# Kernel tuning notes

Measured on AMD Instinct MI355X. Metric: run time of the kernel, lower is better.

## Reference

```python
import jax, jax.numpy as jnp
import numpy as np
from jax import lax

B, T = 2048, 256
H1, H2 = 51, 51


def _cell(x, h, c, w_ih, w_hh, b_ih, b_hh):
    # PyTorch LSTMCell math: gates = x W_ih^T + h W_hh^T + b_ih + b_hh
    gates = x @ w_ih.T + h @ w_hh.T + (b_ih + b_hh)
    i, f, g, o = jnp.split(gates, 4, axis=-1)
    c2 = jax.nn.sigmoid(f) * c + jax.nn.sigmoid(i) * jnp.tanh(g)
    h2 = jax.nn.sigmoid(o) * jnp.tanh(c2)
    return h2, c2


def setup_inputs() -> dict:
    key = jax.random.key(0)
    ks = jax.random.split(key, 17)
    s1 = 1.0 / np.sqrt(H1)
    s4 = 1.0  # hidden size 1 -> bound 1
    def u(k, shape, s):
        return jax.random.uniform(k, shape, jnp.float32, -s, s)
    return {
        "input": jax.random.normal(ks[0], (B, T), jnp.float32),
        "w_ih1": u(ks[1], (4 * H1, 1), s1), "w_hh1": u(ks[2], (4 * H1, H1), s1),
        "b_ih1": u(ks[3], (4 * H1,), s1), "b_hh1": u(ks[4], (4 * H1,), s1),
        "w_ih2": u(ks[5], (4 * H2, H1), s1), "w_hh2": u(ks[6], (4 * H2, H2), s1),
        "b_ih2": u(ks[7], (4 * H2,), s1), "b_hh2": u(ks[8], (4 * H2,), s1),
        "w_ih3": u(ks[9], (4 * H1, H2), s1), "w_hh3": u(ks[10], (4 * H1, H1), s1),
        "b_ih3": u(ks[11], (4 * H1,), s1), "b_hh3": u(ks[12], (4 * H1,), s1),
        "w_ih4": u(ks[13], (4, H1), s4), "w_hh4": u(ks[14], (4, 1), s4),
        "b_ih4": u(ks[15], (4,), s4), "b_hh4": u(ks[16], (4,), s4),
    }


def reference(input, w_ih1, w_hh1, b_ih1, b_hh1, w_ih2, w_hh2, b_ih2, b_hh2,
              w_ih3, w_hh3, b_ih3, b_hh3, w_ih4, w_hh4, b_ih4, b_hh4):
    b = input.shape[0]
    z = lambda d: jnp.zeros((b, d), input.dtype)
    init = (z(H1), z(H1), z(H2), z(H2), z(H1), z(H1), z(1), z(1))

    def stack(x, carry):
        h1, c1, h2, c2, h3, c3, h4, c4 = carry
        h1, c1 = _cell(x, h1, c1, w_ih1, w_hh1, b_ih1, b_hh1)
        # quirk of the original module: cell states feed the next layer
        h2, c2 = _cell(c1, h2, c2, w_ih2, w_hh2, b_ih2, b_hh2)
        h3, c3 = _cell(c2, h3, c3, w_ih3, w_hh3, b_ih3, b_hh3)
        h4, c4 = _cell(c3, h4, c4, w_ih4, w_hh4, b_ih4, b_hh4)
        return (h1, c1, h2, c2, h3, c3, h4, c4)

    def step(carry, x_t):
        return stack(x_t, carry), None

    xs = input.T[:, :, None]  # [T, B, 1]
    carry, _ = lax.scan(step, init, xs)
    # extra step: feed final c4 back as the input
    carry = stack(carry[7], carry)
    return carry[7]  # final cell state of lstm4, shape [B, 1]
```

## Files before the change

### kernel.cpp

```cpp
#include <hip/hip_runtime.h>


typedef _Float16 f16x8 __attribute__((ext_vector_type(8)));
typedef float    f32x4 __attribute__((ext_vector_type(4)));

constexpr int BATCH   = 2048;
constexpr int T_STEPS = 256;
constexpr int H   = 51;
constexpr int NTILE = 13;
constexpr int NUNIT = 5 * NTILE * 2 + 2;
constexpr int XKP = 80;

__device__ __forceinline__ float frcp(float x) { return __builtin_amdgcn_rcpf(x); }
__device__ __forceinline__ float sigmoid_f(float x) { float e = __expf(-x); return frcp(1.f + e); }
__device__ __forceinline__ float tanh_f(float x) {
    float e = __expf(2.f * x);
    return 1.f - 2.f * frcp(e + 1.f);
}

#define PIN16(x) { f32x4 _t = __builtin_bit_cast(f32x4, x); asm volatile("" : "+v"(_t)); x = __builtin_bit_cast(f16x8, _t); }
#define PIN4(x)  asm volatile("" : "+v"(x))

__global__ __launch_bounds__(256) void prep_mfma(
    const float* __restrict__ w_ih1, const float* __restrict__ w_hh1,
    const float* __restrict__ w_ih2, const float* __restrict__ w_hh2,
    const float* __restrict__ w_ih3, const float* __restrict__ w_hh3,
    const float* __restrict__ w_ih4, _Float16* __restrict__ wpa)
{
    int id = blockIdx.x * 256 + threadIdx.x;
    if (id >= NUNIT * 64) return;
    int u = id >> 6, l = id & 63;
    int row16 = l & 15;
    int kbase = ((u & 1) ? 32 : 0) + ((l >> 4) << 3);
    f16x8 v;
    if (u < 130) {
        int pm = u / 26, tile = (u % 26) >> 1;
        const float* W = (pm == 0) ? w_hh1 : (pm == 1) ? w_ih2 : (pm == 2) ? w_hh2
                       : (pm == 3) ? w_ih3 : w_hh3;
        int kh = tile * 4 + (row16 >> 2);
        int q  = row16 & 3;
        bool rv = (kh < H);
        int orow = q * H + kh;
#pragma unroll
        for (int e = 0; e < 8; ++e) {
            int j = kbase + e;
            float val = 0.f;
            if (rv) {
                if (j < H)                  val = W[orow * H + j];
                else if (j == H && pm == 0) val = w_ih1[orow];
            }
            v[e] = (_Float16)val;
        }
    } else {
#pragma unroll
        for (int e = 0; e < 8; ++e) {
            int j = kbase + e;
            v[e] = (_Float16)((row16 < 4 && j < H) ? w_ih4[row16 * H + j] : 0.f);
        }
    }
    *(f16x8*)(wpa + (size_t)u * 512 + l * 8) = v;
}

__global__ __launch_bounds__(512, 2) void lstm4_main(
    const float* __restrict__ input, const _Float16* __restrict__ wpa,
    const float* __restrict__ b_ih1, const float* __restrict__ b_hh1,
    const float* __restrict__ b_ih2, const float* __restrict__ b_hh2,
    const float* __restrict__ b_ih3, const float* __restrict__ b_hh3,
    const float* __restrict__ w_hh4,
    const float* __restrict__ b_ih4, const float* __restrict__ b_hh4,
    float* __restrict__ out)
{
    __shared__ __align__(16) _Float16 xh[6][2][8][XKP];
    __shared__ float inl[8 * 260];

    const int tid  = threadIdx.x;
    const int wave = tid >> 6;
    const int lane = tid & 63;
    const int col  = lane & 15;
    const int rg   = lane >> 4;
    const int bcol = lane & 7;

    const int tile0 = wave;
    const int tile1 = (wave < 5) ? (8 + wave) : wave;
    const bool two  = (wave < 5);
    auto LF = [&](int pm, int tile, int kf) -> f16x8 {
        int u = (pm * NTILE + tile) * 2 + kf;
        return *(const f16x8*)(wpa + (size_t)u * 512 + lane * 8);
    };
    f16x8 fA_0k0  = LF(0, tile0, 0), fA_0k1  = LF(0, tile0, 1);
    f16x8 fA_1k0  = LF(0, tile1, 0), fA_1k1  = LF(0, tile1, 1);
    f16x8 fI2_0k0 = LF(1, tile0, 0), fI2_0k1 = LF(1, tile0, 1);
    f16x8 fI2_1k0 = LF(1, tile1, 0), fI2_1k1 = LF(1, tile1, 1);
    f16x8 fH2_0k0 = LF(2, tile0, 0), fH2_0k1 = LF(2, tile0, 1);
    f16x8 fH2_1k0 = LF(2, tile1, 0), fH2_1k1 = LF(2, tile1, 1);
    f16x8 fI3_0k0 = LF(3, tile0, 0), fI3_0k1 = LF(3, tile0, 1);
    f16x8 fI3_1k0 = LF(3, tile1, 0), fI3_1k1 = LF(3, tile1, 1);
    f16x8 fH3_0k0 = LF(4, tile0, 0), fH3_0k1 = LF(4, tile0, 1);
    f16x8 fH3_1k0 = LF(4, tile1, 0), fH3_1k1 = LF(4, tile1, 1);
    f16x8 fL4k0 = *(const f16x8*)(wpa + (size_t)130 * 512 + lane * 8);
    f16x8 fL4k1 = *(const f16x8*)(wpa + (size_t)131 * 512 + lane * 8);
    PIN16(fA_0k0);  PIN16(fA_0k1);  PIN16(fA_1k0);  PIN16(fA_1k1);
    PIN16(fI2_0k0); PIN16(fI2_0k1); PIN16(fI2_1k0); PIN16(fI2_1k1);
    PIN16(fH2_0k0); PIN16(fH2_0k1); PIN16(fH2_1k0); PIN16(fH2_1k1);
    PIN16(fI3_0k0); PIN16(fI3_0k1); PIN16(fI3_1k0); PIN16(fI3_1k1);
    PIN16(fH3_0k0); PIN16(fH3_0k1); PIN16(fH3_1k0); PIN16(fH3_1k1);
    PIN16(fL4k0);   PIN16(fL4k1);

    const int k0 = tile0 * 4 + rg;
    const int k1 = tile1 * 4 + rg;
    const bool k1v = two && (k1 < H);
    f32x4 cb1v0, cb1v1, cb2v0, cb2v1, cb3v0, cb3v1;
#pragma unroll
    for (int q = 0; q < 4; ++q) {
        cb1v0[q] = b_ih1[q * H + k0] + b_hh1[q * H + k0];
        cb2v0[q] = b_ih2[q * H + k0] + b_hh2[q * H + k0];
        cb3v0[q] = b_ih3[q * H + k0] + b_hh3[q * H + k0];
        cb1v1[q] = k1v ? (b_ih1[q * H + k1] + b_hh1[q * H + k1]) : 0.f;
        cb2v1[q] = k1v ? (b_ih2[q * H + k1] + b_hh2[q * H + k1]) : 0.f;
        cb3v1[q] = k1v ? (b_ih3[q * H + k1] + b_hh3[q * H + k1]) : 0.f;
    }
    PIN4(cb1v0); PIN4(cb1v1); PIN4(cb2v0); PIN4(cb2v1); PIN4(cb3v0); PIN4(cb3v1);
    float bias4v[4], whh4v[4];
#pragma unroll
    for (int q = 0; q < 4; ++q) {
        bias4v[q] = b_ih4[q] + b_hh4[q];
        whh4v[q]  = w_hh4[q];
    }

    {
        const float4 iv = *(const float4*)(input + (size_t)blockIdx.x * 2048 + tid * 4);
        *(float4*)(inl + (tid >> 6) * 260 + (tid & 63) * 4) = iv;
    }
    for (int i = tid; i < 6 * 2 * 8 * XKP; i += 512) ((_Float16*)xh)[i] = (_Float16)0.f;
    __syncthreads();
    if (tid < 8) xh[0][1][tid][H] = (_Float16)inl[tid * 260];
    __syncthreads();

    float c1s = 0.f, c2s = 0.f, c3s = 0.f;
    float h4 = 0.f, c4 = 0.f;

    auto mm = [](f16x8 A, f16x8 B, f32x4 C) {
        return __builtin_amdgcn_mfma_f32_16x16x32_f16(A, B, C, 0, 0, 0);
    };
    auto BF = [&](int v, int p, int kb) -> f16x8 {
        return *(const f16x8*)&xh[v][p][bcol][kb * 32 + rg * 8];
    };
    auto AS = [&](f32x4 a0, f32x4 a1, float& cs, int vh, int vc, int wp) {
        f32x4 a;
#pragma unroll
        for (int q = 0; q < 4; ++q) a[q] = (col < 8) ? a0[q] : a1[q];
        const float i_ = sigmoid_f(a[0]), f_ = sigmoid_f(a[1]);
        const float g_ = tanh_f(a[2]),    o_ = sigmoid_f(a[3]);
        cs = f_ * cs + i_ * g_;
        const float h = o_ * tanh_f(cs);
        const bool st = (col < 8) ? true : (two && k1 < H);
        const int kk = (col < 8) ? k0 : k1;
        if (st) {
            xh[vh][wp][col & 7][kk] = (_Float16)h;
            xh[vc][wp][col & 7][kk] = (_Float16)cs;
        }
    };
    auto L4FIN = [&](f32x4 la) {
        if (lane < 8) {
            const float i_ = sigmoid_f(la[0] + bias4v[0] + whh4v[0] * h4);
            const float f_ = sigmoid_f(la[1] + bias4v[1] + whh4v[1] * h4);
            const float g_ = tanh_f  (la[2] + bias4v[2] + whh4v[2] * h4);
            const float o_ = sigmoid_f(la[3] + bias4v[3] + whh4v[3] * h4);
            c4 = f_ * c4 + i_ * g_;
            h4 = o_ * tanh_f(c4);
        }
    };

    auto runL1 = [&](int rp, int wp) {
        f16x8 b0 = BF(0, rp, 0), b1 = BF(0, rp, 1);
        f32x4 a0 = mm(fA_0k0, b0, cb1v0); a0 = mm(fA_0k1, b1, a0);
        f32x4 a1 = cb1v1;
        if (two) { a1 = mm(fA_1k0, b0, a1); a1 = mm(fA_1k1, b1, a1); }
        AS(a0, a1, c1s, 0, 1, wp);
    };
    auto runL2 = [&](int rx, int rh, int wp) {
        f16x8 x0 = BF(1, rx, 0), x1 = BF(1, rx, 1);
        f16x8 h0 = BF(2, rh, 0), h1f = BF(2, rh, 1);
        f32x4 a0 = mm(fH2_0k0, h0, cb2v0); a0 = mm(fH2_0k1, h1f, a0);
        a0 = mm(fI2_0k0, x0, a0); a0 = mm(fI2_0k1, x1, a0);
        f32x4 a1 = cb2v1;
        if (two) {
            a1 = mm(fH2_1k0, h0, a1); a1 = mm(fH2_1k1, h1f, a1);
            a1 = mm(fI2_1k0, x0, a1); a1 = mm(fI2_1k1, x1, a1);
        }
        AS(a0, a1, c2s, 2, 3, wp);
    };
    auto runL3 = [&](int rx, int rh, int wp) {
        f16x8 x0 = BF(3, rx, 0), x1 = BF(3, rx, 1);
        f16x8 h0 = BF(4, rh, 0), h1f = BF(4, rh, 1);
        f32x4 a0 = mm(fH3_0k0, h0, cb3v0); a0 = mm(fH3_0k1, h1f, a0);
        a0 = mm(fI3_0k0, x0, a0); a0 = mm(fI3_0k1, x1, a0);
        f32x4 a1 = cb3v1;
        if (two) {
            a1 = mm(fH3_1k0, h0, a1); a1 = mm(fH3_1k1, h1f, a1);
            a1 = mm(fI3_1k0, x0, a1); a1 = mm(fI3_1k1, x1, a1);
        }
        AS(a0, a1, c3s, 4, 5, wp);
    };
    auto runL4 = [&](int rp) {
        if (wave == 7) {
            f16x8 b0 = BF(5, rp, 0), b1 = BF(5, rp, 1);
            f32x4 la = {0.f, 0.f, 0.f, 0.f};
            la = mm(fL4k0, b0, la); la = mm(fL4k1, b1, la);
            L4FIN(la);
        }
    };
    auto stageX = [&](int ph) {
        if (wave == 6 && lane < 8 && ph <= 254)
            xh[0][ph & 1][lane][51] = (_Float16)inl[lane * 260 + ph + 1];
    };

    for (int ph = 0; ph <= 2; ++ph) {
        const int pw = ph & 1;
        runL1(1 - pw, pw);
        if (ph >= 1) runL2(1 - pw, pw, 1 - pw);
        if (ph >= 2) runL3(pw, 1 - pw, pw);
        stageX(ph);
        __syncthreads();
    }

    for (int ph = 3; ph <= 255; ++ph) {
        const int pw = ph & 1;
        f16x8 rA0 = BF(0, 1 - pw, 0), rA1 = BF(0, 1 - pw, 1);
        f16x8 r2x0 = BF(1, 1 - pw, 0), r2x1 = BF(1, 1 - pw, 1);
        f16x8 r2h0 = BF(2, pw, 0),     r2h1 = BF(2, pw, 1);
        f16x8 r3x0 = BF(3, pw, 0),     r3x1 = BF(3, pw, 1);
        f16x8 r3h0 = BF(4, 1 - pw, 0), r3h1 = BF(4, 1 - pw, 1);
        f32x4 a0 = mm(fA_0k0, rA0, cb1v0);  a0 = mm(fA_0k1, rA1, a0);
        f32x4 b0 = mm(fH2_0k0, r2h0, cb2v0); b0 = mm(fH2_0k1, r2h1, b0);
        b0 = mm(fI2_0k0, r2x0, b0);          b0 = mm(fI2_0k1, r2x1, b0);
        f32x4 d0 = mm(fH3_0k0, r3h0, cb3v0); d0 = mm(fH3_0k1, r3h1, d0);
        d0 = mm(fI3_0k0, r3x0, d0);          d0 = mm(fI3_0k1, r3x1, d0);
        f32x4 a1 = cb1v1, b1 = cb2v1, d1 = cb3v1;
        if (wave != 7) {
            a1 = mm(fA_1k0, rA0, a1);  a1 = mm(fA_1k1, rA1, a1);
            b1 = mm(fH2_1k0, r2h0, b1); b1 = mm(fH2_1k1, r2h1, b1);
            b1 = mm(fI2_1k0, r2x0, b1); b1 = mm(fI2_1k1, r2x1, b1);
            d1 = mm(fH3_1k0, r3h0, d1); d1 = mm(fH3_1k1, r3h1, d1);
            d1 = mm(fI3_1k0, r3x0, d1); d1 = mm(fI3_1k1, r3x1, d1);
        } else {
            f16x8 l0 = BF(5, 1 - pw, 0), l1 = BF(5, 1 - pw, 1);
            f32x4 la = {0.f, 0.f, 0.f, 0.f};
            la = mm(fL4k0, l0, la); la = mm(fL4k1, l1, la);
            L4FIN(la);
        }
        AS(a0, a1, c1s, 0, 1, pw);
        AS(b0, b1, c2s, 2, 3, 1 - pw);
        AS(d0, d1, c3s, 4, 5, pw);
        stageX(ph);
        __syncthreads();
    }

    for (int ph = 256; ph <= 258; ++ph) {
        const int pw = ph & 1;
        if (ph <= 256) runL2(1 - pw, pw, 1 - pw);
        if (ph <= 257) runL3(pw, 1 - pw, pw);
        runL4(1 - pw);
        __syncthreads();
    }

    if (wave == 7 && lane < 8) xh[0][1][lane][51] = (_Float16)c4;
    __syncthreads();
    runL1(1, 0); __syncthreads();
    runL2(0, 1, 0); __syncthreads();
    runL3(0, 1, 0); __syncthreads();
    runL4(0);
    if (wave == 7 && lane < 8) out[blockIdx.x * 8 + lane] = c4;
}

extern "C" void kernel_launch(void* const* d_in, const int* in_sizes, int n_in,
                              void* d_out, int out_size, void* d_ws, size_t ws_size,
                              hipStream_t stream) {
    const float* input = (const float*)d_in[0];
    const float* w_ih1 = (const float*)d_in[1];
    const float* w_hh1 = (const float*)d_in[2];
    const float* b_ih1 = (const float*)d_in[3];
    const float* b_hh1 = (const float*)d_in[4];
    const float* w_ih2 = (const float*)d_in[5];
    const float* w_hh2 = (const float*)d_in[6];
    const float* b_ih2 = (const float*)d_in[7];
    const float* b_hh2 = (const float*)d_in[8];
    const float* w_ih3 = (const float*)d_in[9];
    const float* w_hh3 = (const float*)d_in[10];
    const float* b_ih3 = (const float*)d_in[11];
    const float* b_hh3 = (const float*)d_in[12];
    const float* w_ih4 = (const float*)d_in[13];
    const float* w_hh4 = (const float*)d_in[14];
    const float* b_ih4 = (const float*)d_in[15];
    const float* b_hh4 = (const float*)d_in[16];

    _Float16* wpa = (_Float16*)d_ws;

    hipLaunchKernelGGL(prep_mfma, dim3((NUNIT * 64 + 255) / 256), dim3(256), 0, stream,
                       w_ih1, w_hh1, w_ih2, w_hh2, w_ih3, w_hh3, w_ih4, wpa);

    hipLaunchKernelGGL(lstm4_main, dim3(BATCH / 8), dim3(512), 0, stream,
                       input, wpa,
                       b_ih1, b_hh1, b_ih2, b_hh2, b_ih3, b_hh3,
                       w_hh4, b_ih4, b_hh4,
                       (float*)d_out);
}
```

Baseline: 327.9 us.

## Fuse weight packing into main LSTM kernel and unroll recurrent loop by two

Removes the separate prep kernel and has every block gather and convert its MFMA weight fragments straight from the fp32 weights into registers. This drops one launch and the workspace round trip. The cost is that all 256 blocks now do scattered global loads and conversions in their prologue. The steady-state loop is also unrolled by two so the ping-pong buffer index becomes a compile-time constant, and the L4 branch is restructured around the 'two' predicate.

```diff
diff --git a/kernel.cpp b/kernel.cpp
--- a/kernel.cpp
+++ b/kernel.cpp
@@ -5,10 +5,7 @@
 typedef float    f32x4 __attribute__((ext_vector_type(4)));
 
 constexpr int BATCH   = 2048;
-constexpr int T_STEPS = 256;
 constexpr int H   = 51;
-constexpr int NTILE = 13;
-constexpr int NUNIT = 5 * NTILE * 2 + 2;
 constexpr int XKP = 80;
 
 __device__ __forceinline__ float frcp(float x) { return __builtin_amdgcn_rcpf(x); }
@@ -21,52 +18,15 @@
 #define PIN16(x) { f32x4 _t = __builtin_bit_cast(f32x4, x); asm volatile("" : "+v"(_t)); x = __builtin_bit_cast(f16x8, _t); }
 #define PIN4(x)  asm volatile("" : "+v"(x))
 
-__global__ __launch_bounds__(256) void prep_mfma(
+__global__ __launch_bounds__(512, 2) void lstm4_main(
+    const float* __restrict__ input,
     const float* __restrict__ w_ih1, const float* __restrict__ w_hh1,
+    const float* __restrict__ b_ih1, const float* __restrict__ b_hh1,
     const float* __restrict__ w_ih2, const float* __restrict__ w_hh2,
+    const float* __restrict__ b_ih2, const float* __restrict__ b_hh2,
     const float* __restrict__ w_ih3, const float* __restrict__ w_hh3,
-    const float* __restrict__ w_ih4, _Float16* __restrict__ wpa)
-{
-    int id = blockIdx.x * 256 + threadIdx.x;
-    if (id >= NUNIT * 64) return;
-    int u = id >> 6, l = id & 63;
-    int row16 = l & 15;
-    int kbase = ((u & 1) ? 32 : 0) + ((l >> 4) << 3);
-    f16x8 v;
-    if (u < 130) {
-        int pm = u / 26, tile = (u % 26) >> 1;
-        const float* W = (pm == 0) ? w_hh1 : (pm == 1) ? w_ih2 : (pm == 2) ? w_hh2
-                       : (pm == 3) ? w_ih3 : w_hh3;
-        int kh = tile * 4 + (row16 >> 2);
-        int q  = row16 & 3;
-        bool rv = (kh < H);
-        int orow = q * H + kh;
-#pragma unroll
-        for (int e = 0; e < 8; ++e) {
-            int j = kbase + e;
-            float val = 0.f;
-            if (rv) {
-                if (j < H)                  val = W[orow * H + j];
-                else if (j == H && pm == 0) val = w_ih1[orow];
-            }
-            v[e] = (_Float16)val;
-        }
-    } else {
-#pragma unroll
-        for (int e = 0; e < 8; ++e) {
-            int j = kbase + e;
-            v[e] = (_Float16)((row16 < 4 && j < H) ? w_ih4[row16 * H + j] : 0.f);
-        }
-    }
-    *(f16x8*)(wpa + (size_t)u * 512 + l * 8) = v;
-}
-
-__global__ __launch_bounds__(512, 2) void lstm4_main(
-    const float* __restrict__ input, const _Float16* __restrict__ wpa,
-    const float* __restrict__ b_ih1, const float* __restrict__ b_hh1,
-    const float* __restrict__ b_ih2, const float* __restrict__ b_hh2,
     const float* __restrict__ b_ih3, const float* __restrict__ b_hh3,
-    const float* __restrict__ w_hh4,
+    const float* __restrict__ w_ih4, const float* __restrict__ w_hh4,
     const float* __restrict__ b_ih4, const float* __restrict__ b_hh4,
     float* __restrict__ out)
 {
@@ -83,22 +43,49 @@
     const int tile0 = wave;
     const int tile1 = (wave < 5) ? (8 + wave) : wave;
     const bool two  = (wave < 5);
-    auto LF = [&](int pm, int tile, int kf) -> f16x8 {
-        int u = (pm * NTILE + tile) * 2 + kf;
-        return *(const f16x8*)(wpa + (size_t)u * 512 + lane * 8);
-    };
-    f16x8 fA_0k0  = LF(0, tile0, 0), fA_0k1  = LF(0, tile0, 1);
-    f16x8 fA_1k0  = LF(0, tile1, 0), fA_1k1  = LF(0, tile1, 1);
-    f16x8 fI2_0k0 = LF(1, tile0, 0), fI2_0k1 = LF(1, tile0, 1);
-    f16x8 fI2_1k0 = LF(1, tile1, 0), fI2_1k1 = LF(1, tile1, 1);
-    f16x8 fH2_0k0 = LF(2, tile0, 0), fH2_0k1 = LF(2, tile0, 1);
-    f16x8 fH2_1k0 = LF(2, tile1, 0), fH2_1k1 = LF(2, tile1, 1);
-    f16x8 fI3_0k0 = LF(3, tile0, 0), fI3_0k1 = LF(3, tile0, 1);
-    f16x8 fI3_1k0 = LF(3, tile1, 0), fI3_1k1 = LF(3, tile1, 1);
-    f16x8 fH3_0k0 = LF(4, tile0, 0), fH3_0k1 = LF(4, tile0, 1);
-    f16x8 fH3_1k0 = LF(4, tile1, 0), fH3_1k1 = LF(4, tile1, 1);
-    f16x8 fL4k0 = *(const f16x8*)(wpa + (size_t)130 * 512 + lane * 8);
-    f16x8 fL4k1 = *(const f16x8*)(wpa + (size_t)131 * 512 + lane * 8);
+
+    auto BUILD = [&](const float* W, const float* xcol, int tile, int kf) -> f16x8 {
+        const int row16 = lane & 15, kgrp = lane >> 4;
+        const int kbase = kf * 32 + kgrp * 8;
+        const int kh = tile * 4 + (row16 >> 2);
+        const int q  = row16 & 3;
+        const int orow = q * H + kh;
+        f16x8 v;
+#pragma unroll
+        for (int e = 0; e < 8; ++e) {
+            const int j = kbase + e;
+            float val = 0.f;
+            if (kh < H) {
+                if (j < H)             val = W[orow * H + j];
+                else if (j == H && xcol) val = xcol[orow];
+            }
+            v[e] = (_Float16)val;
+        }
+        return v;
+    };
+    auto BUILD4 = [&](int kf) -> f16x8 {
+        const int row16 = lane & 15, kgrp = lane >> 4;
+        const int kbase = kf * 32 + kgrp * 8;
+        f16x8 v;
+#pragma unroll
+        for (int e = 0; e < 8; ++e) {
+            const int j = kbase + e;
+            v[e] = (_Float16)((row16 < 4 && j < H) ? w_ih4[row16 * H + j] : 0.f);
+        }
+        return v;
+    };
+
+    f16x8 fA_0k0  = BUILD(w_hh1, w_ih1, tile0, 0), fA_0k1  = BUILD(w_hh1, w_ih1, tile0, 1);
+    f16x8 fA_1k0  = BUILD(w_hh1, w_ih1, tile1, 0), fA_1k1  = BUILD(w_hh1, w_ih1, tile1, 1);
+    f16x8 fI2_0k0 = BUILD(w_ih2, nullptr, tile0, 0), fI2_0k1 = BUILD(w_ih2, nullptr, tile0, 1);
+    f16x8 fI2_1k0 = BUILD(w_ih2, nullptr, tile1, 0), fI2_1k1 = BUILD(w_ih2, nullptr, tile1, 1);
+    f16x8 fH2_0k0 = BUILD(w_hh2, nullptr, tile0, 0), fH2_0k1 = BUILD(w_hh2, nullptr, tile0, 1);
+    f16x8 fH2_1k0 = BUILD(w_hh2, nullptr, tile1, 0), fH2_1k1 = BUILD(w_hh2, nullptr, tile1, 1);
+    f16x8 fI3_0k0 = BUILD(w_ih3, nullptr, tile0, 0), fI3_0k1 = BUILD(w_ih3, nullptr, tile0, 1);
+    f16x8 fI3_1k0 = BUILD(w_ih3, nullptr, tile1, 0), fI3_1k1 = BUILD(w_ih3, nullptr, tile1, 1);
+    f16x8 fH3_0k0 = BUILD(w_hh3, nullptr, tile0, 0), fH3_0k1 = BUILD(w_hh3, nullptr, tile0, 1);
+    f16x8 fH3_1k0 = BUILD(w_hh3, nullptr, tile1, 0), fH3_1k1 = BUILD(w_hh3, nullptr, tile1, 1);
+    f16x8 fL4k0 = BUILD4(0), fL4k1 = BUILD4(1);
     PIN16(fA_0k0);  PIN16(fA_0k1);  PIN16(fA_1k0);  PIN16(fA_1k1);
     PIN16(fI2_0k0); PIN16(fI2_0k1); PIN16(fI2_1k0); PIN16(fI2_1k1);
     PIN16(fH2_0k0); PIN16(fH2_0k1); PIN16(fH2_1k0); PIN16(fH2_1k1);
@@ -215,6 +202,37 @@
             xh[0][ph & 1][lane][51] = (_Float16)inl[lane * 260 + ph + 1];
     };
 
+    auto STEP = [&](int pw, int ph) {
+        f16x8 rA0 = BF(0, 1 - pw, 0), rA1 = BF(0, 1 - pw, 1);
+        f16x8 r2x0 = BF(1, 1 - pw, 0), r2x1 = BF(1, 1 - pw, 1);
+        f16x8 r2h0 = BF(2, pw, 0),     r2h1 = BF(2, pw, 1);
+        f16x8 r3x0 = BF(3, pw, 0),     r3x1 = BF(3, pw, 1);
+        f16x8 r3h0 = BF(4, 1 - pw, 0), r3h1 = BF(4, 1 - pw, 1);
+        f32x4 a0 = mm(fA_0k0, rA0, cb1v0);   a0 = mm(fA_0k1, rA1, a0);
+        f32x4 b0 = mm(fH2_0k0, r2h0, cb2v0); b0 = mm(fH2_0k1, r2h1, b0);
+        b0 = mm(fI2_0k0, r2x0, b0);          b0 = mm(fI2_0k1, r2x1, b0);
+        f32x4 d0 = mm(fH3_0k0, r3h0, cb3v0); d0 = mm(fH3_0k1, r3h1, d0);
+        d0 = mm(fI3_0k0, r3x0, d0);          d0 = mm(fI3_0k1, r3x1, d0);
+        f32x4 a1 = cb1v1, b1 = cb2v1, d1 = cb3v1;
+        if (two) {
+            a1 = mm(fA_1k0, rA0, a1);   a1 = mm(fA_1k1, rA1, a1);
+            b1 = mm(fH2_1k0, r2h0, b1); b1 = mm(fH2_1k1, r2h1, b1);
+            b1 = mm(fI2_1k0, r2x0, b1); b1 = mm(fI2_1k1, r2x1, b1);
+            d1 = mm(fH3_1k0, r3h0, d1); d1 = mm(fH3_1k1, r3h1, d1);
+            d1 = mm(fI3_1k0, r3x0, d1); d1 = mm(fI3_1k1, r3x1, d1);
+        } else if (wave == 7) {
+            f16x8 l0 = BF(5, 1 - pw, 0), l1 = BF(5, 1 - pw, 1);
+            f32x4 la = {0.f, 0.f, 0.f, 0.f};
+            la = mm(fL4k0, l0, la); la = mm(fL4k1, l1, la);
+            L4FIN(la);
+        }
+        AS(a0, a1, c1s, 0, 1, pw);
+        AS(b0, b1, c2s, 2, 3, 1 - pw);
+        AS(d0, d1, c3s, 4, 5, pw);
+        stageX(ph);
+        __syncthreads();
+    };
+
     for (int ph = 0; ph <= 2; ++ph) {
         const int pw = ph & 1;
         runL1(1 - pw, pw);
@@ -224,37 +242,11 @@
         __syncthreads();
     }
 
-    for (int ph = 3; ph <= 255; ++ph) {
-        const int pw = ph & 1;
-        f16x8 rA0 = BF(0, 1 - pw, 0), rA1 = BF(0, 1 - pw, 1);
-        f16x8 r2x0 = BF(1, 1 - pw, 0), r2x1 = BF(1, 1 - pw, 1);
-        f16x8 r2h0 = BF(2, pw, 0),     r2h1 = BF(2, pw, 1);
-        f16x8 r3x0 = BF(3, pw, 0),     r3x1 = BF(3, pw, 1);
-        f16x8 r3h0 = BF(4, 1 - pw, 0), r3h1 = BF(4, 1 - pw, 1);
-        f32x4 a0 = mm(fA_0k0, rA0, cb1v0);  a0 = mm(fA_0k1, rA1, a0);
-        f32x4 b0 = mm(fH2_0k0, r2h0, cb2v0); b0 = mm(fH2_0k1, r2h1, b0);
-        b0 = mm(fI2_0k0, r2x0, b0);          b0 = mm(fI2_0k1, r2x1, b0);
-        f32x4 d0 = mm(fH3_0k0, r3h0, cb3v0); d0 = mm(fH3_0k1, r3h1, d0);
-        d0 = mm(fI3_0k0, r3x0, d0);          d0 = mm(fI3_0k1, r3x1, d0);
-        f32x4 a1 = cb1v1, b1 = cb2v1, d1 = cb3v1;
-        if (wave != 7) {
-            a1 = mm(fA_1k0, rA0, a1);  a1 = mm(fA_1k1, rA1, a1);
-            b1 = mm(fH2_1k0, r2h0, b1); b1 = mm(fH2_1k1, r2h1, b1);
-            b1 = mm(fI2_1k0, r2x0, b1); b1 = mm(fI2_1k1, r2x1, b1);
-            d1 = mm(fH3_1k0, r3h0, d1); d1 = mm(fH3_1k1, r3h1, d1);
-            d1 = mm(fI3_1k0, r3x0, d1); d1 = mm(fI3_1k1, r3x1, d1);
-        } else {
-            f16x8 l0 = BF(5, 1 - pw, 0), l1 = BF(5, 1 - pw, 1);
-            f32x4 la = {0.f, 0.f, 0.f, 0.f};
-            la = mm(fL4k0, l0, la); la = mm(fL4k1, l1, la);
-            L4FIN(la);
-        }
-        AS(a0, a1, c1s, 0, 1, pw);
-        AS(b0, b1, c2s, 2, 3, 1 - pw);
-        AS(d0, d1, c3s, 4, 5, pw);
-        stageX(ph);
-        __syncthreads();
-    }
+    for (int ph = 3; ph <= 253; ph += 2) {
+        STEP(1, ph);
+        STEP(0, ph + 1);
+    }
+    STEP(1, 255);
 
     for (int ph = 256; ph <= 258; ++ph) {
         const int pw = ph & 1;
@@ -294,14 +286,11 @@
     const float* b_ih4 = (const float*)d_in[15];
     const float* b_hh4 = (const float*)d_in[16];
 
-    _Float16* wpa = (_Float16*)d_ws;
-
-    hipLaunchKernelGGL(prep_mfma, dim3((NUNIT * 64 + 255) / 256), dim3(256), 0, stream,
-                       w_ih1, w_hh1, w_ih2, w_hh2, w_ih3, w_hh3, w_ih4, wpa);
-
     hipLaunchKernelGGL(lstm4_main, dim3(BATCH / 8), dim3(512), 0, stream,
-                       input, wpa,
-                       b_ih1, b_hh1, b_ih2, b_hh2, b_ih3, b_hh3,
-                       w_hh4, b_ih4, b_hh4,
+                       input,
+                       w_ih1, w_hh1, b_ih1, b_hh1,
+                       w_ih2, w_hh2, b_ih2, b_hh2,
+                       w_ih3, w_hh3, b_ih3, b_hh3,
+                       w_ih4, w_hh4, b_ih4, b_hh4,
                        (float*)d_out);
 }
```

After: 333.4 us. No clear change (+1.7%).
